# Kernel tuning notes

Measured on AMD Instinct MI355X. Metric: run time of the kernel, lower is better.

Reference implementation:

```python
import jax, jax.numpy as jnp
import numpy as np

EPS = 1e-8  # torch F.cosine_similarity eps


def setup_inputs() -> dict:
    key = jax.random.key(0)
    ks = jax.random.split(key, 5)
    S, Q, D_in, D, N_WAY, K_SHOT = 100, 4096, 21168, 64, 20, 5
    return {
        "support_images": jax.random.normal(ks[0], (S, D_in), dtype=jnp.float32),
        "support_labels": jax.random.randint(ks[1], (S,), 0, N_WAY),
        "query_images": jax.random.normal(ks[2], (Q, D_in), dtype=jnp.float32),
        "n_way": N_WAY,
        "k_shot": K_SHOT,
        "backbone_w": jax.random.normal(ks[3], (D_in, D), dtype=jnp.float32) * 0.02,
        "backbone_b": jax.random.normal(ks[4], (D,), dtype=jnp.float32) * 0.02,
    }


def _l2_normalize(x):
    # matches torch cosine_similarity: x / max(||x||, eps)
    n = jnp.maximum(jnp.linalg.norm(x, axis=-1, keepdims=True), EPS)
    return x / n


def reference(support_images, support_labels, query_images, n_way, k_shot,
              backbone_w, backbone_b):
    # Backbone: linear embedding (stand-in for conv feature extractor)
    support_emb = support_images @ backbone_w + backbone_b   # [S, D]
    query_emb = query_images @ backbone_w + backbone_b       # [Q, D]

    # Cosine similarity between every query and every support sample: [Q, S]
    sims = _l2_normalize(query_emb) @ _l2_normalize(support_emb).T

    # Softmax over the support axis (per query), as in the original loop
    attn = jax.nn.softmax(sims, axis=1)                      # [Q, S]

    # Per-label scatter-add == one-hot segment-sum: [Q, n_way]
    one_hot = jax.nn.one_hot(support_labels, n_way, dtype=attn.dtype)  # [S, n_way]
    logits = attn @ one_hot
    return logits
```

## Files before the change

### kernel.cpp

```cpp
#include <hip/hip_runtime.h>
#include <hip/hip_bf16.h>
#include <math.h>

#define DEMB 64
#define BM   64
#define KSMAX 16

using short8 = __attribute__((ext_vector_type(8))) short;
using u16x8  = __attribute__((ext_vector_type(8))) unsigned short;
using f32x4  = __attribute__((ext_vector_type(4))) float;

__device__ __forceinline__ unsigned short f2bf(float x) {
    union { float f; unsigned u; } v; v.f = x;
    unsigned r = v.u + 0x7fffu + ((v.u >> 16) & 1u);
    return (unsigned short)(r >> 16);
}

__global__ __launch_bounds__(256) void prep_wt(
    const float* __restrict__ W, unsigned short* __restrict__ Wt,
    int Din, int Wstride)
{
    __shared__ unsigned short tile[64][65];
    const int k0 = blockIdx.x * 64;
    const int tid = threadIdx.x;
    #pragma unroll
    for (int i = 0; i < 16; ++i) {
        int kk = i * 4 + (tid >> 6);
        int c  = tid & 63;
        int k  = k0 + kk;
        float x = (k < Din) ? W[(size_t)k * DEMB + c] : 0.f;
        tile[kk][c] = f2bf(x);
    }
    __syncthreads();
    #pragma unroll
    for (int i = 0; i < 16; ++i) {
        int c  = i * 4 + (tid >> 6);
        int kk = tid & 63;
        Wt[(size_t)c * Wstride + k0 + kk] = tile[kk][c];
    }
}

__global__ __launch_bounds__(256) void gemm_mfma(
    const float* __restrict__ Xq, const float* __restrict__ Xs,
    const unsigned short* __restrict__ Wt,
    float* __restrict__ qpart, float* __restrict__ spart,
    int Q, int S, int Din, int Wstride, int nQb, int ks)
{
    __shared__ unsigned short As[2][BM * 32];
    __shared__ unsigned short Ws[2][64 * 32];

    const int tid  = threadIdx.x;
    const int wave = tid >> 6;
    const int lane = tid & 63;
    const int kg   = blockIdx.y;

    const bool isS = (int)blockIdx.x >= nQb;
    const float* X = isS ? Xs : Xq;
    const int nrows = isS ? S : Q;
    const int r0 = (isS ? ((int)blockIdx.x - nQb) : (int)blockIdx.x) * BM;
    float* part = isS ? spart : qpart;
    const int prow = isS ? 128 : Q;

    const int arow = tid >> 2;
    const int ak   = (tid & 3) * 8;
    const bool aval = (r0 + arow) < nrows;
    const float* aptr = X + (size_t)(r0 + arow) * Din;

    const unsigned short* wptr = Wt + (size_t)(tid >> 2) * Wstride + (tid & 3) * 8;

    const int frow = 16 * wave + (lane & 15);
    const int fk   = (lane >> 4) * 8;

    f32x4 acc[4] = { {0.f,0.f,0.f,0.f}, {0.f,0.f,0.f,0.f},
                     {0.f,0.f,0.f,0.f}, {0.f,0.f,0.f,0.f} };

    const int nchunk = (Din + 31) >> 5;

    {
        const int k0 = kg * 32;
        float4 a0 = {}, a1 = {};
        const int kk = k0 + ak;
        if (aval && kk + 8 <= Din) {
            a0 = *reinterpret_cast<const float4*>(aptr + kk);
            a1 = *reinterpret_cast<const float4*>(aptr + kk + 4);
        }
        u16x8 wv = *reinterpret_cast<const u16x8*>(wptr + k0);
        u16x8 ap = { f2bf(a0.x), f2bf(a0.y), f2bf(a0.z), f2bf(a0.w),
                     f2bf(a1.x), f2bf(a1.y), f2bf(a1.z), f2bf(a1.w) };
        *reinterpret_cast<u16x8*>(&As[0][arow * 32 + ak]) = ap;
        *reinterpret_cast<u16x8*>(&Ws[0][tid * 8]) = wv;
        __syncthreads();
    }

    int cur = 0;
    for (int c = kg; c < nchunk; c += ks) {
        const int cn = c + ks;
        const bool pf = (cn < nchunk);
        float4 a0 = {}, a1 = {};
        u16x8 wv = {0,0,0,0,0,0,0,0};
        if (pf) {
            const int k0 = cn * 32;
            const int kk = k0 + ak;
            if (aval && kk + 8 <= Din) {
                a0 = *reinterpret_cast<const float4*>(aptr + kk);
                a1 = *reinterpret_cast<const float4*>(aptr + kk + 4);
            }
            wv = *reinterpret_cast<const u16x8*>(wptr + k0);
        }

        short8 af = *reinterpret_cast<const short8*>(&As[cur][frow * 32 + fk]);
        #pragma unroll
        for (int cb = 0; cb < 4; ++cb) {
            short8 bf = *reinterpret_cast<const short8*>(
                &Ws[cur][(16 * cb + (lane & 15)) * 32 + fk]);
            acc[cb] = __builtin_amdgcn_mfma_f32_16x16x32_bf16(af, bf, acc[cb], 0, 0, 0);
        }

        if (pf) {
            u16x8 ap = { f2bf(a0.x), f2bf(a0.y), f2bf(a0.z), f2bf(a0.w),
                         f2bf(a1.x), f2bf(a1.y), f2bf(a1.z), f2bf(a1.w) };
            *reinterpret_cast<u16x8*>(&As[cur ^ 1][arow * 32 + ak]) = ap;
            *reinterpret_cast<u16x8*>(&Ws[cur ^ 1][tid * 8]) = wv;
        }
        __syncthreads();
        cur ^= 1;
    }

    #pragma unroll
    for (int cb = 0; cb < 4; ++cb) {
        #pragma unroll
        for (int i = 0; i < 4; ++i) {
            int row = r0 + 16 * wave + (lane >> 4) * 4 + i;
            if (row < nrows)
                part[((size_t)kg * prow + row) * DEMB + 16 * cb + (lane & 15)] = acc[cb][i];
        }
    }
}

__global__ void support_finalize(const float* __restrict__ spart,
                                 const float* __restrict__ bias,
                                 float* __restrict__ sn, int S, int ks)
{
    int s = blockIdx.x;
    int c = threadIdx.x;
    float e = bias[c];
    for (int g = 0; g < ks; ++g)
        e += spart[((size_t)g * 128 + s) * DEMB + c];
    float ss = e * e;
    #pragma unroll
    for (int o = 32; o >= 1; o >>= 1) ss += __shfl_xor(ss, o, 64);
    sn[(size_t)s * DEMB + c] = e / fmaxf(sqrtf(ss), 1e-8f);
}

__global__ __launch_bounds__(256) void attend(
    const float* __restrict__ qpart, const float* __restrict__ sn_g,
    const float* __restrict__ bias, const int* __restrict__ labels,
    const int* __restrict__ p_nway, float* __restrict__ out,
    int S, int Q, int ks)
{
    __shared__ float sn[100][65];
    __shared__ float qn[4][64];
    __shared__ float bins[4][32];
    __shared__ int   lab[100];

    const int tid  = threadIdx.x;
    const int w    = tid >> 6;
    const int lane = tid & 63;
    const int nw   = *p_nway;

    for (int i = tid; i < S * DEMB; i += 256) sn[i >> 6][i & 63] = sn_g[i];
    if (tid < S) lab[tid] = labels[tid];

    const int q = blockIdx.x * 4 + w;

    float e = bias[lane];
    for (int g = 0; g < ks; ++g)
        e += qpart[((size_t)g * Q + q) * DEMB + lane];
    float ss = e * e;
    #pragma unroll
    for (int o = 32; o >= 1; o >>= 1) ss += __shfl_xor(ss, o, 64);
    e /= fmaxf(sqrtf(ss), 1e-8f);
    qn[w][lane] = e;
    if (lane < 32) bins[w][lane] = 0.f;
    __syncthreads();

    const bool v1 = (lane + 64) < S;
    const int  s1 = v1 ? lane + 64 : 0;
    float sim0 = 0.f, sim1 = 0.f;
    #pragma unroll 8
    for (int c = 0; c < DEMB; ++c) {
        float qc = qn[w][c];
        sim0 += qc * sn[lane][c];
        sim1 += qc * sn[s1][c];
    }
    if (!v1) sim1 = -INFINITY;

    float lm = fmaxf(sim0, sim1);
    #pragma unroll
    for (int o = 32; o >= 1; o >>= 1) lm = fmaxf(lm, __shfl_xor(lm, o, 64));
    float e0 = __expf(sim0 - lm);
    float e1 = v1 ? __expf(sim1 - lm) : 0.f;
    float d = e0 + e1;
    #pragma unroll
    for (int o = 32; o >= 1; o >>= 1) d += __shfl_xor(d, o, 64);

    atomicAdd(&bins[w][lab[lane]], e0);
    if (v1) atomicAdd(&bins[w][lab[s1]], e1);
    __syncthreads();

    if (lane < nw) out[(size_t)q * nw + lane] = bins[w][lane] / d;
}

extern "C" void kernel_launch(void* const* d_in, const int* in_sizes, int n_in,
                              void* d_out, int out_size, void* d_ws, size_t ws_size,
                              hipStream_t stream)
{
    const float* sup    = (const float*)d_in[0];
    const int*   labels = (const int*)d_in[1];
    const float* qry    = (const float*)d_in[2];
    const int*   p_nway = (const int*)d_in[3];
    const float* W      = (const float*)d_in[5];
    const float* bias   = (const float*)d_in[6];
    float* out = (float*)d_out;

    const int D   = DEMB;
    const int Din = in_sizes[5] / D;
    const int Q   = in_sizes[2] / Din;
    const int S   = in_sizes[1];

    const int nchunk  = (Din + 31) / 32;
    const int Wstride = nchunk * 32;

    char* wsb = (char*)d_ws;
    size_t wt_bytes = (size_t)64 * Wstride * sizeof(unsigned short);
    wt_bytes = (wt_bytes + 255) & ~(size_t)255;
    size_t sn_bytes = (size_t)S * D * sizeof(float);
    sn_bytes = (sn_bytes + 255) & ~(size_t)255;
    size_t per_ks = ((size_t)Q * D + 128 * D) * sizeof(float);

    size_t fixed = wt_bytes + sn_bytes;
    int ks = 1;
    if (ws_size > fixed + per_ks) {
        size_t avail = (ws_size - fixed) / per_ks;
        ks = (int)(avail < KSMAX ? avail : KSMAX);
        if (ks < 1) ks = 1;
    }

    unsigned short* Wt = (unsigned short*)wsb;
    float* sn    = (float*)(wsb + wt_bytes);
    float* spart = (float*)(wsb + wt_bytes + sn_bytes);
    float* qpart = spart + (size_t)ks * 128 * D;

    hipLaunchKernelGGL(prep_wt, dim3((Din + 63) / 64), dim3(256), 0, stream,
                       W, Wt, Din, Wstride);

    const int nQb = (Q + BM - 1) / BM;
    const int nSb = (S + BM - 1) / BM;
    hipLaunchKernelGGL(gemm_mfma, dim3(nQb + nSb, ks), dim3(256), 0, stream,
                       qry, sup, Wt, qpart, spart, Q, S, Din, Wstride, nQb, ks);

    hipLaunchKernelGGL(support_finalize, dim3(S), dim3(64), 0, stream,
                       spart, bias, sn, S, ks);

    hipLaunchKernelGGL(attend, dim3(Q / 4), dim3(256), 0, stream,
                       qpart, sn, bias, labels, p_nway, out, S, Q, ks);
}
```

Baseline: 137.6 us.

## Stream GEMM operands directly from global into MFMA fragments without LDS staging

Rewrites the split-K GEMM so each lane loads its A and W fragments straight from global memory into registers and feeds the MFMA, dropping the LDS double buffer and the per-chunk barriers. Each K-group now covers a contiguous range of chunks instead of an interleaved stride, and the maximum split count rises to 24. Launch bounds now request 4 blocks per CU, and bf16 conversion uses the intrinsic. W fragments are read repeatedly from global/L2 with less coalesced access, and the larger split count adds more partial-sum traffic in the reductions.

```diff
diff --git a/kernel.cpp b/kernel.cpp
--- a/kernel.cpp
+++ b/kernel.cpp
@@ -4,16 +4,28 @@
 
 #define DEMB 64
 #define BM   64
-#define KSMAX 16
+#define KSMAX 24
 
 using short8 = __attribute__((ext_vector_type(8))) short;
-using u16x8  = __attribute__((ext_vector_type(8))) unsigned short;
 using f32x4  = __attribute__((ext_vector_type(4))) float;
 
 __device__ __forceinline__ unsigned short f2bf(float x) {
     union { float f; unsigned u; } v; v.f = x;
     unsigned r = v.u + 0x7fffu + ((v.u >> 16) & 1u);
     return (unsigned short)(r >> 16);
+}
+
+__device__ __forceinline__ short8 cvt_bf8(float4 a0, float4 a1) {
+    union { short8 s; __hip_bfloat16 h[8]; } u;
+    u.h[0] = __float2bfloat16(a0.x);
+    u.h[1] = __float2bfloat16(a0.y);
+    u.h[2] = __float2bfloat16(a0.z);
+    u.h[3] = __float2bfloat16(a0.w);
+    u.h[4] = __float2bfloat16(a1.x);
+    u.h[5] = __float2bfloat16(a1.y);
+    u.h[6] = __float2bfloat16(a1.z);
+    u.h[7] = __float2bfloat16(a1.w);
+    return u.s;
 }
 
 __global__ __launch_bounds__(256) void prep_wt(
@@ -40,15 +52,12 @@
     }
 }
 
-__global__ __launch_bounds__(256) void gemm_mfma(
+__global__ __launch_bounds__(256, 4) void gemm_stream(
     const float* __restrict__ Xq, const float* __restrict__ Xs,
     const unsigned short* __restrict__ Wt,
     float* __restrict__ qpart, float* __restrict__ spart,
-    int Q, int S, int Din, int Wstride, int nQb, int ks)
-{
-    __shared__ unsigned short As[2][BM * 32];
-    __shared__ unsigned short Ws[2][64 * 32];
-
+    int Q, int S, int Din, int Wstride, int nQb, int cpk, int nchunk)
+{
     const int tid  = threadIdx.x;
     const int wave = tid >> 6;
     const int lane = tid & 63;
@@ -57,73 +66,52 @@
     const bool isS = (int)blockIdx.x >= nQb;
     const float* X = isS ? Xs : Xq;
     const int nrows = isS ? S : Q;
-    const int r0 = (isS ? ((int)blockIdx.x - nQb) : (int)blockIdx.x) * BM;
+    const int r0 = (isS ? (int)blockIdx.x - nQb : (int)blockIdx.x) * BM;
     float* part = isS ? spart : qpart;
     const int prow = isS ? 128 : Q;
 
-    const int arow = tid >> 2;
-    const int ak   = (tid & 3) * 8;
-    const bool aval = (r0 + arow) < nrows;
-    const float* aptr = X + (size_t)(r0 + arow) * Din;
-
-    const unsigned short* wptr = Wt + (size_t)(tid >> 2) * Wstride + (tid & 3) * 8;
-
-    const int frow = 16 * wave + (lane & 15);
-    const int fk   = (lane >> 4) * 8;
+    int arow = r0 + 16 * wave + (lane & 15);
+    if (arow >= nrows) arow = nrows - 1;
+    const int fk = (lane >> 4) * 8;
+    const float* aptr = X + (size_t)arow * Din + fk;
+    const unsigned short* bptr = Wt + (size_t)(lane & 15) * Wstride + fk;
 
     f32x4 acc[4] = { {0.f,0.f,0.f,0.f}, {0.f,0.f,0.f,0.f},
                      {0.f,0.f,0.f,0.f}, {0.f,0.f,0.f,0.f} };
 
-    const int nchunk = (Din + 31) >> 5;
-
-    {
-        const int k0 = kg * 32;
-        float4 a0 = {}, a1 = {};
-        const int kk = k0 + ak;
-        if (aval && kk + 8 <= Din) {
-            a0 = *reinterpret_cast<const float4*>(aptr + kk);
-            a1 = *reinterpret_cast<const float4*>(aptr + kk + 4);
-        }
-        u16x8 wv = *reinterpret_cast<const u16x8*>(wptr + k0);
-        u16x8 ap = { f2bf(a0.x), f2bf(a0.y), f2bf(a0.z), f2bf(a0.w),
-                     f2bf(a1.x), f2bf(a1.y), f2bf(a1.z), f2bf(a1.w) };
-        *reinterpret_cast<u16x8*>(&As[0][arow * 32 + ak]) = ap;
-        *reinterpret_cast<u16x8*>(&Ws[0][tid * 8]) = wv;
-        __syncthreads();
-    }
-
-    int cur = 0;
-    for (int c = kg; c < nchunk; c += ks) {
-        const int cn = c + ks;
-        const bool pf = (cn < nchunk);
-        float4 a0 = {}, a1 = {};
-        u16x8 wv = {0,0,0,0,0,0,0,0};
-        if (pf) {
-            const int k0 = cn * 32;
-            const int kk = k0 + ak;
-            if (aval && kk + 8 <= Din) {
-                a0 = *reinterpret_cast<const float4*>(aptr + kk);
-                a1 = *reinterpret_cast<const float4*>(aptr + kk + 4);
-            }
-            wv = *reinterpret_cast<const u16x8*>(wptr + k0);
-        }
-
-        short8 af = *reinterpret_cast<const short8*>(&As[cur][frow * 32 + fk]);
+    const int c0    = kg * cpk;
+    const int c1    = (c0 + cpk < nchunk) ? c0 + cpk : nchunk;
+    const int cfull = Din >> 5;
+    const int c1f   = (c1 < cfull) ? c1 : cfull;
+
+    #pragma unroll 2
+    for (int c = c0; c < c1f; ++c) {
+        const int k0 = c * 32;
+        float4 a0 = *reinterpret_cast<const float4*>(aptr + k0);
+        float4 a1 = *reinterpret_cast<const float4*>(aptr + k0 + 4);
+        short8 af = cvt_bf8(a0, a1);
         #pragma unroll
         for (int cb = 0; cb < 4; ++cb) {
             short8 bf = *reinterpret_cast<const short8*>(
-                &Ws[cur][(16 * cb + (lane & 15)) * 32 + fk]);
+                bptr + (size_t)cb * 16 * Wstride + k0);
             acc[cb] = __builtin_amdgcn_mfma_f32_16x16x32_bf16(af, bf, acc[cb], 0, 0, 0);
         }
-
-        if (pf) {
-            u16x8 ap = { f2bf(a0.x), f2bf(a0.y), f2bf(a0.z), f2bf(a0.w),
-                         f2bf(a1.x), f2bf(a1.y), f2bf(a1.z), f2bf(a1.w) };
-            *reinterpret_cast<u16x8*>(&As[cur ^ 1][arow * 32 + ak]) = ap;
-            *reinterpret_cast<u16x8*>(&Ws[cur ^ 1][tid * 8]) = wv;
-        }
-        __syncthreads();
-        cur ^= 1;
+    }
+
+    if (c1 > c1f) {
+        const int k0 = c1f * 32;
+        float4 a0 = {0.f,0.f,0.f,0.f}, a1 = {0.f,0.f,0.f,0.f};
+        if (k0 + fk + 8 <= Din) {
+            a0 = *reinterpret_cast<const float4*>(aptr + k0);
+            a1 = *reinterpret_cast<const float4*>(aptr + k0 + 4);
+        }
+        short8 af = cvt_bf8(a0, a1);
+        #pragma unroll
+        for (int cb = 0; cb < 4; ++cb) {
+            short8 bf = *reinterpret_cast<const short8*>(
+                bptr + (size_t)cb * 16 * Wstride + k0);
+            acc[cb] = __builtin_amdgcn_mfma_f32_16x16x32_bf16(af, bf, acc[cb], 0, 0, 0);
+        }
     }
 
     #pragma unroll
@@ -139,12 +127,12 @@
 
 __global__ void support_finalize(const float* __restrict__ spart,
                                  const float* __restrict__ bias,
-                                 float* __restrict__ sn, int S, int ks)
+                                 float* __restrict__ sn, int S, int nkg)
 {
     int s = blockIdx.x;
     int c = threadIdx.x;
     float e = bias[c];
-    for (int g = 0; g < ks; ++g)
+    for (int g = 0; g < nkg; ++g)
         e += spart[((size_t)g * 128 + s) * DEMB + c];
     float ss = e * e;
     #pragma unroll
@@ -156,7 +144,7 @@
     const float* __restrict__ qpart, const float* __restrict__ sn_g,
     const float* __restrict__ bias, const int* __restrict__ labels,
     const int* __restrict__ p_nway, float* __restrict__ out,
-    int S, int Q, int ks)
+    int S, int Q, int nkg)
 {
     __shared__ float sn[100][65];
     __shared__ float qn[4][64];
@@ -174,7 +162,7 @@
     const int q = blockIdx.x * 4 + w;
 
     float e = bias[lane];
-    for (int g = 0; g < ks; ++g)
+    for (int g = 0; g < nkg; ++g)
         e += qpart[((size_t)g * Q + q) * DEMB + lane];
     float ss = e * e;
     #pragma unroll
@@ -245,23 +233,25 @@
         ks = (int)(avail < KSMAX ? avail : KSMAX);
         if (ks < 1) ks = 1;
     }
+    const int cpk = (nchunk + ks - 1) / ks;
+    const int nkg = (nchunk + cpk - 1) / cpk;
 
     unsigned short* Wt = (unsigned short*)wsb;
     float* sn    = (float*)(wsb + wt_bytes);
     float* spart = (float*)(wsb + wt_bytes + sn_bytes);
-    float* qpart = spart + (size_t)ks * 128 * D;
+    float* qpart = spart + (size_t)nkg * 128 * D;
 
     hipLaunchKernelGGL(prep_wt, dim3((Din + 63) / 64), dim3(256), 0, stream,
                        W, Wt, Din, Wstride);
 
     const int nQb = (Q + BM - 1) / BM;
     const int nSb = (S + BM - 1) / BM;
-    hipLaunchKernelGGL(gemm_mfma, dim3(nQb + nSb, ks), dim3(256), 0, stream,
-                       qry, sup, Wt, qpart, spart, Q, S, Din, Wstride, nQb, ks);
+    hipLaunchKernelGGL(gemm_stream, dim3(nQb + nSb, nkg), dim3(256), 0, stream,
+                       qry, sup, Wt, qpart, spart, Q, S, Din, Wstride, nQb, cpk, nchunk);
 
     hipLaunchKernelGGL(support_finalize, dim3(S), dim3(64), 0, stream,
-                       spart, bias, sn, S, ks);
+                       spart, bias, sn, S, nkg);
 
     hipLaunchKernelGGL(attend, dim3(Q / 4), dim3(256), 0, stream,
-                       qpart, sn, bias, labels, p_nway, out, S, Q, ks);
-}
+                       qpart, sn, bias, labels, p_nway, out, S, Q, nkg);
+}
```

After: 185.3 us. 1.35x slower.
